# Performance work log

Hardware: AMD Instinct MI355X
Metric: run time of the kernel (lower is better)

Reference implementation:

```python
import jax, jax.numpy as jnp
import numpy as np


def setup_inputs() -> dict:
    key = jax.random.key(0)
    kq, kk, kv, kmask = jax.random.split(key, 4)
    B, H, L, D = 2, 16, 2048, 64
    q = jax.random.normal(kq, (B, H, L, D), dtype=jnp.float32)
    k = jax.random.normal(kk, (B, H, L, D), dtype=jnp.float32)
    v = jax.random.normal(kv, (B, H, L, D), dtype=jnp.float32)
    valid = jax.random.randint(kmask, (B, H, L, L), 0, 2, dtype=jnp.int32)
    scale = jnp.ones((), dtype=jnp.float32)  # typically 1/sqrt(D)
    return {"q": q, "k": k, "v": v, "valid": valid, "scale": scale}


def reference(q, k, v, valid, scale):
    # scores: [B, H, Lq, Lk]
    att_v = jnp.einsum('bhqd,bhkd->bhqk', q, k)
    att_v = att_v * scale
    att_v = att_v - jnp.max(att_v, axis=-1, keepdims=True)
    att_v = jnp.where(valid <= 0, -jnp.inf, att_v)
    att_w = jax.nn.softmax(att_v, axis=-1)
    # rows that are fully masked produce NaN -> zero them (matches torch masked_fill on isnan)
    att_w = jnp.where(jnp.isnan(att_w), jnp.zeros((), dtype=att_w.dtype), att_w)
    result = jnp.einsum('bhqk,bhkd->bhqd', att_w, v)
    return (result, att_w)
```

## Files before the change

### kernel.cpp

```cpp
#include <hip/hip_runtime.h>
#include <hip/hip_bf16.h>

#define B_    2
#define H_    16
#define L_    2048
#define D_    64
#define QT    64
#define KTILE 64
#define NKT   (L_ / KTILE)
#define PITCH 72
#define VPITCH 70
#define MPITCH 132

typedef __bf16 bf16x8 __attribute__((ext_vector_type(8)));
typedef float  f32x4  __attribute__((ext_vector_type(4)));

__device__ __forceinline__ f32x4 mfma16(bf16x8 a, bf16x8 b, f32x4 c) {
    return __builtin_amdgcn_mfma_f32_16x16x32_bf16(a, b, c, 0, 0, 0);
}

__global__ __launch_bounds__(256)
void attn_fused(const float* __restrict__ Qg, const float* __restrict__ Kg,
                const float* __restrict__ Vg, const int* __restrict__ validg,
                const float* __restrict__ scaleg,
                float* __restrict__ outR, float* __restrict__ outW)
{
    __shared__ __attribute__((aligned(16))) __bf16 KbufH[KTILE][PITCH];
    __shared__ __attribute__((aligned(16))) __bf16 KbufL[KTILE][PITCH];
    __shared__ __attribute__((aligned(16))) __bf16 Vbuf[KTILE][VPITCH];
    __shared__ __attribute__((aligned(16))) __bf16 Pbuf[QT][PITCH];
    __shared__ unsigned short Mask[QT][MPITCH];

    const int tid  = threadIdx.x;
    const int wv   = tid >> 6;
    const int lane = tid & 63;
    const int ln   = lane & 15;
    const int qd   = lane >> 4;

    const int bidx = blockIdx.x;
    const int bh   = (bidx & 7) * 4 + ((bidx >> 3) & 3);
    const int qt   = bidx >> 5;

    const float scale = scaleg[0];

    const float* Qb = Qg + ((size_t)bh * L_ + (size_t)qt * QT) * D_;
    const float* Kb = Kg + (size_t)bh * L_ * D_;
    const float* Vb = Vg + (size_t)bh * L_ * D_;
    const int*   Mb = validg + ((size_t)bh * L_ + (size_t)qt * QT) * (size_t)L_;
    float* Ob = outR + ((size_t)bh * L_ + (size_t)qt * QT) * D_;
    float* Wb = outW + ((size_t)bh * L_ + (size_t)qt * QT) * (size_t)L_;

    bf16x8 aH[2], aL[2];
    {
        const float* qrow = Qb + (size_t)(wv * 16 + ln) * D_;
#pragma unroll
        for (int f = 0; f < 2; ++f) {
            f32x4 x0 = *(const f32x4*)(qrow + f * 32 + qd * 8);
            f32x4 x1 = *(const f32x4*)(qrow + f * 32 + qd * 8 + 4);
            bf16x8 h, l;
#pragma unroll
            for (int j = 0; j < 4; ++j) {
                float v0 = x0[j], v1 = x1[j];
                __bf16 h0 = (__bf16)v0, h1 = (__bf16)v1;
                h[j] = h0; h[4 + j] = h1;
                l[j]     = (__bf16)(v0 - (float)h0);
                l[4 + j] = (__bf16)(v1 - (float)h1);
            }
            aH[f] = h; aL[f] = l;
        }
    }

    const int sr = tid >> 2;
    const int sc = (tid & 3) * 16;

    auto stageK = [&](int kt) {
        const float* src = Kb + (size_t)(kt * KTILE + sr) * D_ + sc;
        f32x4 w0 = *(const f32x4*)(src);
        f32x4 w1 = *(const f32x4*)(src + 4);
        f32x4 w2 = *(const f32x4*)(src + 8);
        f32x4 w3 = *(const f32x4*)(src + 12);
        bf16x8 h0, h1, l0, l1;
#pragma unroll
        for (int j = 0; j < 4; ++j) {
            { float v = w0[j]; __bf16 h = (__bf16)v; h0[j]   = h; l0[j]   = (__bf16)(v - (float)h); }
            { float v = w1[j]; __bf16 h = (__bf16)v; h0[4+j] = h; l0[4+j] = (__bf16)(v - (float)h); }
            { float v = w2[j]; __bf16 h = (__bf16)v; h1[j]   = h; l1[j]   = (__bf16)(v - (float)h); }
            { float v = w3[j]; __bf16 h = (__bf16)v; h1[4+j] = h; l1[4+j] = (__bf16)(v - (float)h); }
        }
        *(bf16x8*)&KbufH[sr][sc]     = h0;
        *(bf16x8*)&KbufH[sr][sc + 8] = h1;
        *(bf16x8*)&KbufL[sr][sc]     = l0;
        *(bf16x8*)&KbufL[sr][sc + 8] = l1;
    };

    float lsum[4] = {0.f, 0.f, 0.f, 0.f};

    for (int kt = 0; kt < NKT; ++kt) {
        __syncthreads();
        stageK(kt);
        {
            const int* src = Mb + (size_t)sr * L_ + kt * KTILE + sc;
            int vals[16];
            *(int4*)(vals)      = *(const int4*)(src);
            *(int4*)(vals + 4)  = *(const int4*)(src + 4);
            *(int4*)(vals + 8)  = *(const int4*)(src + 8);
            *(int4*)(vals + 12) = *(const int4*)(src + 12);
            unsigned m = 0;
#pragma unroll
            for (int i = 0; i < 16; ++i) m |= (unsigned)(vals[i] > 0) << i;
            Mask[sr][kt * 4 + (tid & 3)] = (unsigned short)m;
        }
        __syncthreads();
#pragma unroll
        for (int ct = 0; ct < 4; ++ct) {
            const int kr = ct * 16 + ln;
            bf16x8 bh0 = *(const bf16x8*)&KbufH[kr][qd * 8];
            bf16x8 bh1 = *(const bf16x8*)&KbufH[kr][32 + qd * 8];
            bf16x8 bl0 = *(const bf16x8*)&KbufL[kr][qd * 8];
            bf16x8 bl1 = *(const bf16x8*)&KbufL[kr][32 + qd * 8];
            f32x4 acc = {0.f, 0.f, 0.f, 0.f};
            acc = mfma16(aL[0], bh0, acc);
            acc = mfma16(aL[1], bh1, acc);
            acc = mfma16(aH[0], bl0, acc);
            acc = mfma16(aH[1], bl1, acc);
            acc = mfma16(aH[0], bh0, acc);
            acc = mfma16(aH[1], bh1, acc);
#pragma unroll
            for (int r = 0; r < 4; ++r) {
                unsigned mb = Mask[wv * 16 + qd * 4 + r][kt * 4 + ct];
                float bit = (float)((mb >> ln) & 1u);
                lsum[r] += bit * __expf(acc[r] * scale);
            }
        }
    }

    float invl[4];
#pragma unroll
    for (int r = 0; r < 4; ++r) {
        float v = lsum[r];
        v += __shfl_xor(v, 1);
        v += __shfl_xor(v, 2);
        v += __shfl_xor(v, 4);
        v += __shfl_xor(v, 8);
        invl[r] = v > 0.f ? 1.f / v : 0.f;
    }

    f32x4 accO[4];
#pragma unroll
    for (int i = 0; i < 4; ++i) accO[i] = (f32x4){0.f, 0.f, 0.f, 0.f};

    for (int kt = 0; kt < NKT; ++kt) {
        __syncthreads();
        stageK(kt);
        {
            const float* src = Vb + (size_t)(kt * KTILE + sr) * D_ + sc;
            float tv[16];
            *(f32x4*)(tv)      = *(const f32x4*)(src);
            *(f32x4*)(tv + 4)  = *(const f32x4*)(src + 4);
            *(f32x4*)(tv + 8)  = *(const f32x4*)(src + 8);
            *(f32x4*)(tv + 12) = *(const f32x4*)(src + 12);
#pragma unroll
            for (int i = 0; i < 8; ++i) {
                __bf16 b0 = (__bf16)tv[2 * i], b1 = (__bf16)tv[2 * i + 1];
                unsigned packed = ((unsigned)*(unsigned short*)&b1 << 16) | *(unsigned short*)&b0;
                *(unsigned*)&Vbuf[sr][sc + 2 * i] = packed;
            }
        }
        __syncthreads();
#pragma unroll
        for (int ct = 0; ct < 4; ++ct) {
            const int kr = ct * 16 + ln;
            bf16x8 bh0 = *(const bf16x8*)&KbufH[kr][qd * 8];
            bf16x8 bh1 = *(const bf16x8*)&KbufH[kr][32 + qd * 8];
            bf16x8 bl0 = *(const bf16x8*)&KbufL[kr][qd * 8];
            bf16x8 bl1 = *(const bf16x8*)&KbufL[kr][32 + qd * 8];
            f32x4 acc = {0.f, 0.f, 0.f, 0.f};
            acc = mfma16(aL[0], bh0, acc);
            acc = mfma16(aL[1], bh1, acc);
            acc = mfma16(aH[0], bl0, acc);
            acc = mfma16(aH[1], bl1, acc);
            acc = mfma16(aH[0], bh0, acc);
            acc = mfma16(aH[1], bh1, acc);
#pragma unroll
            for (int r = 0; r < 4; ++r) {
                const int qrow = wv * 16 + qd * 4 + r;
                unsigned mb = Mask[qrow][kt * 4 + ct];
                float bit = (float)((mb >> ln) & 1u);
                float p = bit * __expf(acc[r] * scale) * invl[r];
                Wb[(size_t)qrow * L_ + (size_t)(kt * KTILE + ct * 16 + ln)] = p;
                Pbuf[qrow][ct * 16 + ln] = (__bf16)p;
            }
        }
        bf16x8 p0 = *(const bf16x8*)&Pbuf[wv * 16 + ln][qd * 8];
        bf16x8 p1 = *(const bf16x8*)&Pbuf[wv * 16 + ln][32 + qd * 8];
#pragma unroll
        for (int c2 = 0; c2 < 4; ++c2) {
            bf16x8 v0, v1;
#pragma unroll
            for (int j = 0; j < 8; ++j) {
                v0[j] = Vbuf[qd * 8 + j][c2 * 16 + ln];
                v1[j] = Vbuf[32 + qd * 8 + j][c2 * 16 + ln];
            }
            accO[c2] = mfma16(p0, v0, accO[c2]);
            accO[c2] = mfma16(p1, v1, accO[c2]);
        }
    }

#pragma unroll
    for (int c2 = 0; c2 < 4; ++c2)
#pragma unroll
        for (int r = 0; r < 4; ++r)
            Ob[(size_t)(wv * 16 + qd * 4 + r) * D_ + (c2 * 16 + ln)] = accO[c2][r];
}

extern "C" void kernel_launch(void* const* d_in, const int* in_sizes, int n_in,
                              void* d_out, int out_size, void* d_ws, size_t ws_size,
                              hipStream_t stream) {
    const float* q     = (const float*)d_in[0];
    const float* k     = (const float*)d_in[1];
    const float* v     = (const float*)d_in[2];
    const int*   valid = (const int*)d_in[3];
    const float* scale = (const float*)d_in[4];

    float* out_res  = (float*)d_out;
    float* out_attw = out_res + (size_t)B_ * H_ * L_ * D_;

    dim3 grid(B_ * H_ * (L_ / QT));
    dim3 block(256);
    attn_fused<<<grid, block, 0, stream>>>(q, k, v, valid, scale, out_res, out_attw);
}
```

Measured before the change: 1.181 ms.

## Switch attention to single fp16 MFMA, direct-to-LDS K loads, register masks

Replaces the split bf16 hi/lo QK^T (six MFMAs per tile) with a single fp16 MFMA pass, and loads K as raw fp32 straight into LDS through global_load_lds, converting to fp16 at fragment read. The mask is read per lane in the first pass and kept as bits in registers for the second pass, which removes the shared mask buffer. V is stored transposed and swizzled so fragments load as vectors, attention weights go out as 128-bit stores read back from the P buffer, and launch bounds ask for four blocks per CU. The risk is precision: fp16 scores with scale=1 and unbounded logits lose accuracy, the unnormalised exp can overflow, and the attention weights written out are rounded to fp16.

```diff
diff --git a/kernel.cpp b/kernel.cpp
--- a/kernel.cpp
+++ b/kernel.cpp
@@ -1,35 +1,32 @@
 #include <hip/hip_runtime.h>
 #include <hip/hip_bf16.h>
-
-#define B_    2
-#define H_    16
+#include <hip/hip_fp16.h>
+
 #define L_    2048
 #define D_    64
 #define QT    64
-#define KTILE 64
-#define NKT   (L_ / KTILE)
-#define PITCH 72
-#define VPITCH 70
-#define MPITCH 132
-
-typedef __bf16 bf16x8 __attribute__((ext_vector_type(8)));
-typedef float  f32x4  __attribute__((ext_vector_type(4)));
-
-__device__ __forceinline__ f32x4 mfma16(bf16x8 a, bf16x8 b, f32x4 c) {
-    return __builtin_amdgcn_mfma_f32_16x16x32_bf16(a, b, c, 0, 0, 0);
+#define NKT   32
+#define KGPITCH 260
+#define VTP   72
+#define PBP   72
+
+typedef _Float16 half8 __attribute__((ext_vector_type(8)));
+typedef _Float16 half2v __attribute__((ext_vector_type(2)));
+typedef float    f32x4 __attribute__((ext_vector_type(4)));
+
+__device__ __forceinline__ f32x4 mfma16f(half8 a, half8 b, f32x4 c) {
+    return __builtin_amdgcn_mfma_f32_16x16x32_f16(a, b, c, 0, 0, 0);
 }
 
-__global__ __launch_bounds__(256)
+__global__ __launch_bounds__(256, 4)
 void attn_fused(const float* __restrict__ Qg, const float* __restrict__ Kg,
                 const float* __restrict__ Vg, const int* __restrict__ validg,
                 const float* __restrict__ scaleg,
                 float* __restrict__ outR, float* __restrict__ outW)
 {
-    __shared__ __attribute__((aligned(16))) __bf16 KbufH[KTILE][PITCH];
-    __shared__ __attribute__((aligned(16))) __bf16 KbufL[KTILE][PITCH];
-    __shared__ __attribute__((aligned(16))) __bf16 Vbuf[KTILE][VPITCH];
-    __shared__ __attribute__((aligned(16))) __bf16 Pbuf[QT][PITCH];
-    __shared__ unsigned short Mask[QT][MPITCH];
+    __shared__ __attribute__((aligned(16))) float    Klds[16 * KGPITCH];
+    __shared__ __attribute__((aligned(16))) _Float16 Vt[64 * VTP];
+    __shared__ __attribute__((aligned(16))) _Float16 Pbuf[64 * PBP];
 
     const int tid  = threadIdx.x;
     const int wv   = tid >> 6;
@@ -50,88 +47,78 @@
     float* Ob = outR + ((size_t)bh * L_ + (size_t)qt * QT) * D_;
     float* Wb = outW + ((size_t)bh * L_ + (size_t)qt * QT) * (size_t)L_;
 
-    bf16x8 aH[2], aL[2];
+    half8 aF[2];
     {
         const float* qrow = Qb + (size_t)(wv * 16 + ln) * D_;
 #pragma unroll
         for (int f = 0; f < 2; ++f) {
             f32x4 x0 = *(const f32x4*)(qrow + f * 32 + qd * 8);
             f32x4 x1 = *(const f32x4*)(qrow + f * 32 + qd * 8 + 4);
-            bf16x8 h, l;
-#pragma unroll
-            for (int j = 0; j < 4; ++j) {
-                float v0 = x0[j], v1 = x1[j];
-                __bf16 h0 = (__bf16)v0, h1 = (__bf16)v1;
-                h[j] = h0; h[4 + j] = h1;
-                l[j]     = (__bf16)(v0 - (float)h0);
-                l[4 + j] = (__bf16)(v1 - (float)h1);
-            }
-            aH[f] = h; aL[f] = l;
-        }
-    }
-
-    const int sr = tid >> 2;
-    const int sc = (tid & 3) * 16;
+            half8 h;
+#pragma unroll
+            for (int j = 0; j < 4; ++j) { h[j] = (_Float16)x0[j]; h[4 + j] = (_Float16)x1[j]; }
+            aF[f] = h;
+        }
+    }
 
     auto stageK = [&](int kt) {
-        const float* src = Kb + (size_t)(kt * KTILE + sr) * D_ + sc;
-        f32x4 w0 = *(const f32x4*)(src);
-        f32x4 w1 = *(const f32x4*)(src + 4);
-        f32x4 w2 = *(const f32x4*)(src + 8);
-        f32x4 w3 = *(const f32x4*)(src + 12);
-        bf16x8 h0, h1, l0, l1;
+        const float* gbase = Kb + (size_t)kt * 64 * 64;
+#pragma unroll
+        for (int gi = 0; gi < 4; ++gi) {
+            const int grp = wv * 4 + gi;
+            __builtin_amdgcn_global_load_lds(
+                (const __attribute__((address_space(1))) void*)(gbase + grp * 256 + lane * 4),
+                (__attribute__((address_space(3))) void*)&Klds[grp * KGPITCH],
+                16, 0, 0);
+        }
+    };
+
+    auto kfrags = [&](int kr, half8& b0, half8& b1) {
+        const float* kp = &Klds[(kr >> 2) * KGPITCH + (kr & 3) * 64 + qd * 8];
+        f32x4 x0 = *(const f32x4*)kp;
+        f32x4 x1 = *(const f32x4*)(kp + 4);
+        f32x4 y0 = *(const f32x4*)(kp + 32);
+        f32x4 y1 = *(const f32x4*)(kp + 36);
 #pragma unroll
         for (int j = 0; j < 4; ++j) {
-            { float v = w0[j]; __bf16 h = (__bf16)v; h0[j]   = h; l0[j]   = (__bf16)(v - (float)h); }
-            { float v = w1[j]; __bf16 h = (__bf16)v; h0[4+j] = h; l0[4+j] = (__bf16)(v - (float)h); }
-            { float v = w2[j]; __bf16 h = (__bf16)v; h1[j]   = h; l1[j]   = (__bf16)(v - (float)h); }
-            { float v = w3[j]; __bf16 h = (__bf16)v; h1[4+j] = h; l1[4+j] = (__bf16)(v - (float)h); }
-        }
-        *(bf16x8*)&KbufH[sr][sc]     = h0;
-        *(bf16x8*)&KbufH[sr][sc + 8] = h1;
-        *(bf16x8*)&KbufL[sr][sc]     = l0;
-        *(bf16x8*)&KbufL[sr][sc + 8] = l1;
+            b0[j] = (_Float16)x0[j]; b0[4 + j] = (_Float16)x1[j];
+            b1[j] = (_Float16)y0[j]; b1[4 + j] = (_Float16)y1[j];
+        }
     };
 
+    const int* maskbase = Mb + (size_t)(wv * 16 + qd * 4) * L_ + ln;
+
+    unsigned mreg[16];
+#pragma unroll
+    for (int i = 0; i < 16; ++i) mreg[i] = 0u;
     float lsum[4] = {0.f, 0.f, 0.f, 0.f};
 
     for (int kt = 0; kt < NKT; ++kt) {
         __syncthreads();
         stageK(kt);
-        {
-            const int* src = Mb + (size_t)sr * L_ + kt * KTILE + sc;
-            int vals[16];
-            *(int4*)(vals)      = *(const int4*)(src);
-            *(int4*)(vals + 4)  = *(const int4*)(src + 4);
-            *(int4*)(vals + 8)  = *(const int4*)(src + 8);
-            *(int4*)(vals + 12) = *(const int4*)(src + 12);
-            unsigned m = 0;
-#pragma unroll
-            for (int i = 0; i < 16; ++i) m |= (unsigned)(vals[i] > 0) << i;
-            Mask[sr][kt * 4 + (tid & 3)] = (unsigned short)m;
-        }
-        __syncthreads();
+        int mv[16];
+#pragma unroll
+        for (int ct = 0; ct < 4; ++ct)
+#pragma unroll
+            for (int r = 0; r < 4; ++r)
+                mv[ct * 4 + r] = maskbase[(size_t)r * L_ + kt * 64 + ct * 16];
+        __syncthreads();
+        unsigned bits = 0;
 #pragma unroll
         for (int ct = 0; ct < 4; ++ct) {
-            const int kr = ct * 16 + ln;
-            bf16x8 bh0 = *(const bf16x8*)&KbufH[kr][qd * 8];
-            bf16x8 bh1 = *(const bf16x8*)&KbufH[kr][32 + qd * 8];
-            bf16x8 bl0 = *(const bf16x8*)&KbufL[kr][qd * 8];
-            bf16x8 bl1 = *(const bf16x8*)&KbufL[kr][32 + qd * 8];
+            half8 b0, b1;
+            kfrags(ct * 16 + ln, b0, b1);
             f32x4 acc = {0.f, 0.f, 0.f, 0.f};
-            acc = mfma16(aL[0], bh0, acc);
-            acc = mfma16(aL[1], bh1, acc);
-            acc = mfma16(aH[0], bl0, acc);
-            acc = mfma16(aH[1], bl1, acc);
-            acc = mfma16(aH[0], bh0, acc);
-            acc = mfma16(aH[1], bh1, acc);
+            acc = mfma16f(aF[0], b0, acc);
+            acc = mfma16f(aF[1], b1, acc);
 #pragma unroll
             for (int r = 0; r < 4; ++r) {
-                unsigned mb = Mask[wv * 16 + qd * 4 + r][kt * 4 + ct];
-                float bit = (float)((mb >> ln) & 1u);
-                lsum[r] += bit * __expf(acc[r] * scale);
-            }
-        }
+                unsigned bit = (mv[ct * 4 + r] > 0) ? 1u : 0u;
+                bits |= bit << (ct * 4 + r);
+                lsum[r] += (float)bit * __expf(acc[r] * scale);
+            }
+        }
+        mreg[kt >> 1] |= bits << ((kt & 1) * 16);
     }
 
     float invl[4];
@@ -149,60 +136,68 @@
 #pragma unroll
     for (int i = 0; i < 4; ++i) accO[i] = (f32x4){0.f, 0.f, 0.f, 0.f};
 
+    const int rp = tid >> 3;
+    const int vc = tid & 7;
+    const int dc = vc * 8;
+
     for (int kt = 0; kt < NKT; ++kt) {
         __syncthreads();
         stageK(kt);
         {
-            const float* src = Vb + (size_t)(kt * KTILE + sr) * D_ + sc;
-            float tv[16];
-            *(f32x4*)(tv)      = *(const f32x4*)(src);
-            *(f32x4*)(tv + 4)  = *(const f32x4*)(src + 4);
-            *(f32x4*)(tv + 8)  = *(const f32x4*)(src + 8);
-            *(f32x4*)(tv + 12) = *(const f32x4*)(src + 12);
+            const float* v0p = Vb + ((size_t)kt * 64 + 2 * rp) * 64 + dc;
+            f32x4 va0 = *(const f32x4*)v0p;
+            f32x4 va1 = *(const f32x4*)(v0p + 4);
+            f32x4 vb0 = *(const f32x4*)(v0p + 64);
+            f32x4 vb1 = *(const f32x4*)(v0p + 68);
+            const int g = (rp >> 2) ^ vc;
 #pragma unroll
             for (int i = 0; i < 8; ++i) {
-                __bf16 b0 = (__bf16)tv[2 * i], b1 = (__bf16)tv[2 * i + 1];
-                unsigned packed = ((unsigned)*(unsigned short*)&b1 << 16) | *(unsigned short*)&b0;
-                *(unsigned*)&Vbuf[sr][sc + 2 * i] = packed;
+                float f0 = (i < 4) ? va0[i] : va1[i - 4];
+                float f1 = (i < 4) ? vb0[i] : vb1[i - 4];
+                half2v h; h[0] = (_Float16)f0; h[1] = (_Float16)f1;
+                const int d = dc + i;
+                *(half2v*)&Vt[d * VTP + 8 * g + 2 * (rp & 3)] = h;
             }
         }
         __syncthreads();
 #pragma unroll
         for (int ct = 0; ct < 4; ++ct) {
-            const int kr = ct * 16 + ln;
-            bf16x8 bh0 = *(const bf16x8*)&KbufH[kr][qd * 8];
-            bf16x8 bh1 = *(const bf16x8*)&KbufH[kr][32 + qd * 8];
-            bf16x8 bl0 = *(const bf16x8*)&KbufL[kr][qd * 8];
-            bf16x8 bl1 = *(const bf16x8*)&KbufL[kr][32 + qd * 8];
+            half8 b0, b1;
+            kfrags(ct * 16 + ln, b0, b1);
             f32x4 acc = {0.f, 0.f, 0.f, 0.f};
-            acc = mfma16(aL[0], bh0, acc);
-            acc = mfma16(aL[1], bh1, acc);
-            acc = mfma16(aH[0], bl0, acc);
-            acc = mfma16(aH[1], bl1, acc);
-            acc = mfma16(aH[0], bh0, acc);
-            acc = mfma16(aH[1], bh1, acc);
+            acc = mfma16f(aF[0], b0, acc);
+            acc = mfma16f(aF[1], b1, acc);
 #pragma unroll
             for (int r = 0; r < 4; ++r) {
                 const int qrow = wv * 16 + qd * 4 + r;
-                unsigned mb = Mask[qrow][kt * 4 + ct];
-                float bit = (float)((mb >> ln) & 1u);
+                float bit = (float)((mreg[kt >> 1] >> ((kt & 1) * 16 + ct * 4 + r)) & 1u);
                 float p = bit * __expf(acc[r] * scale) * invl[r];
-                Wb[(size_t)qrow * L_ + (size_t)(kt * KTILE + ct * 16 + ln)] = p;
-                Pbuf[qrow][ct * 16 + ln] = (__bf16)p;
-            }
-        }
-        bf16x8 p0 = *(const bf16x8*)&Pbuf[wv * 16 + ln][qd * 8];
-        bf16x8 p1 = *(const bf16x8*)&Pbuf[wv * 16 + ln][32 + qd * 8];
+                Pbuf[qrow * PBP + ct * 16 + ln] = (_Float16)p;
+            }
+        }
+        half8 p0 = *(const half8*)&Pbuf[(wv * 16 + ln) * PBP + qd * 8];
+        half8 p1 = *(const half8*)&Pbuf[(wv * 16 + ln) * PBP + 32 + qd * 8];
+        {
+            float* wp = Wb + (size_t)(wv * 16 + ln) * L_ + kt * 64;
+            f32x4 s0, s1, s2, s3;
+#pragma unroll
+            for (int j = 0; j < 4; ++j) {
+                s0[j] = (float)p0[j];     s1[j] = (float)p0[4 + j];
+                s2[j] = (float)p1[j];     s3[j] = (float)p1[4 + j];
+            }
+            *(f32x4*)(wp + qd * 8)      = s0;
+            *(f32x4*)(wp + qd * 8 + 4)  = s1;
+            *(f32x4*)(wp + 32 + qd * 8)     = s2;
+            *(f32x4*)(wp + 32 + qd * 8 + 4) = s3;
+        }
 #pragma unroll
         for (int c2 = 0; c2 < 4; ++c2) {
-            bf16x8 v0, v1;
-#pragma unroll
-            for (int j = 0; j < 8; ++j) {
-                v0[j] = Vbuf[qd * 8 + j][c2 * 16 + ln];
-                v1[j] = Vbuf[32 + qd * 8 + j][c2 * 16 + ln];
-            }
-            accO[c2] = mfma16(p0, v0, accO[c2]);
-            accO[c2] = mfma16(p1, v1, accO[c2]);
+            const int d  = c2 * 16 + ln;
+            const int g2 = (d >> 3) & 7;
+            half8 v0 = *(const half8*)&Vt[d * VTP + 8 * (qd ^ g2)];
+            half8 v1 = *(const half8*)&Vt[d * VTP + 8 * ((4 + qd) ^ g2)];
+            accO[c2] = mfma16f(p0, v0, accO[c2]);
+            accO[c2] = mfma16f(p1, v1, accO[c2]);
         }
     }
 
@@ -223,9 +218,9 @@
     const float* scale = (const float*)d_in[4];
 
     float* out_res  = (float*)d_out;
-    float* out_attw = out_res + (size_t)B_ * H_ * L_ * D_;
-
-    dim3 grid(B_ * H_ * (L_ / QT));
+    float* out_attw = out_res + (size_t)2 * 16 * L_ * D_;
+
+    dim3 grid(2 * 16 * (L_ / QT));
     dim3 block(256);
     attn_fused<<<grid, block, 0, stream>>>(q, k, v, valid, scale, out_res, out_attw);
 }
```

New measurement: 1.120 ms. 1.05x faster.
